# Kernel tuning notes

Hardware: AMD Instinct MI355X
Metric: run time of the kernel (lower is better)

## Reference

```python
import jax, jax.numpy as jnp
import numpy as np

N, E, CN, CE = 2048, 8192, 256, 256
MN, ME = 16384, 65536
RATIO = 0.5
K_KEEP = int(np.ceil(RATIO * N))  # 1024, static


def _glorot(key, shape):
    lim = float(np.sqrt(6.0 / (shape[0] + shape[1])))
    return jax.random.uniform(key, shape, jnp.float32, -lim, lim)


def setup_inputs() -> dict:
    key = jax.random.key(0)
    ks = jax.random.split(key, 16)
    return {
        "x_n": jax.random.normal(ks[0], (N, CN), jnp.float32),
        "edge_index_n": jax.random.randint(ks[1], (2, MN), 0, N),
        "edge_weight_n": jax.random.uniform(ks[2], (MN,), jnp.float32),
        "x_e": jax.random.normal(ks[3], (E, CE), jnp.float32),
        "edge_index_e": jax.random.randint(ks[4], (2, ME), 0, E),
        "edge_weight_e": jax.random.uniform(ks[5], (ME,), jnp.float32),
        "edge_index": jax.random.randint(ks[6], (2, E), 0, N),
        "n_batch": jnp.zeros((N,), jnp.int64 if jax.config.jax_enable_x64 else jnp.int32),
        "e_batch": jnp.zeros((E,), jnp.int64 if jax.config.jax_enable_x64 else jnp.int32),
        "x_n0": jax.random.normal(ks[7], (N, CN), jnp.float32),
        "x_e0": jax.random.normal(ks[8], (E, CE), jnp.float32),
        # HodgeLaguerreConv(in, 1, K=2) params for node- and edge-scoring GNNs
        "W_n0": _glorot(ks[9], (CN, 1)),
        "W_n1": _glorot(ks[10], (CN, 1)),
        "b_n": jnp.zeros((1,), jnp.float32),
        "W_e0": _glorot(ks[11], (CE, 1)),
        "W_e1": _glorot(ks[12], (CE, 1)),
        "b_e": jnp.zeros((1,), jnp.float32),
    }


def _hodge_conv_k2(x, ei, ew, W0, W1, b):
    # PyG: out = lin0(T0) + lin1(T1), T0 = x, T1 = x - L@x (propagate: dst += w_e * x[src])
    n = x.shape[0]
    agg = jax.ops.segment_sum(ew[:, None] * x[ei[0]], ei[1], num_segments=n)
    return x @ W0 + (x - agg) @ W1 + b


def reference(x_n, edge_index_n, edge_weight_n, x_e, edge_index_e, edge_weight_e,
              edge_index, n_batch, e_batch, x_n0, x_e0,
              W_n0, W_n1, b_n, W_e0, W_e1, b_e):
    score_n = jax.nn.sigmoid(_hodge_conv_k2(x_n, edge_index_n, edge_weight_n, W_n0, W_n1, b_n).reshape(-1))
    score_e = jax.nn.sigmoid(_hodge_conv_k2(x_e, edge_index_e, edge_weight_e, W_e0, W_e1, b_e).reshape(-1))
    xns = x_n * score_n[:, None]
    xes = x_e * score_e[:, None]
    # incidence matrix B (par1): B[src,e]=-1, B[dst,e]=+1 (duplicates summed, as torch sparse)
    src, dst = edge_index[0], edge_index[1]
    eidx = jnp.arange(E)
    par1 = jnp.zeros((N, E), x_n.dtype).at[src, eidx].add(-1.0).at[dst, eidx].add(1.0)
    par1_abs = jnp.zeros((N, E), x_n.dtype).at[src, eidx].add(1.0).at[dst, eidx].add(1.0)
    # joint node score with 0.125 * |B| @ score_e
    joint = score_n + 0.125 * (par1_abs @ score_e)
    perm = jnp.argsort(-joint)                # descending
    idx_keep = jnp.sort(perm[:K_KEEP])        # kept nodes in original order (boolean-mask order)
    mask_n = jnp.zeros((N,), x_n.dtype).at[idx_keep].set(1.0)
    # edges touching any removed node get nonzero; keep edges where this is exactly 0
    removed_hits = par1_abs.T @ (1.0 - mask_n)
    keep_e = (removed_hits == 0.0).astype(x_n.dtype)     # [E]
    # masked incidence: kept-node rows, removed-edge columns zeroed
    par_masked = par1[idx_keep] * keep_e[None, :]        # [k, E]
    L0 = par_masked @ par_masked.T                       # [k, k]  (equals compacted L0)
    L1 = par_masked.T @ par_masked                       # [E, E]  (zero rows/cols at removed edges)
    # eigsh(L0, k=1, 'LM'): max eigenvalue; scipy path is non-differentiable -> stop_gradient
    lam = jax.lax.stop_gradient(jnp.linalg.eigvalsh(L0)[-1])
    L0s = 2.0 * L0 / lam
    L1s = 2.0 * L1 / lam
    x_n_out = xns[idx_keep]
    x_e_out = xes * keep_e[:, None]
    x_n0_out = x_n0[idx_keep]
    x_e0_out = x_e0 * keep_e[:, None]
    return (x_n_out, L0s, x_e_out, L1s, par_masked, x_n0_out, x_e0_out)
```

## Files before the change

### kernel.cpp

```cpp
#include <hip/hip_runtime.h>
#include <math.h>

#define NN   2048
#define EE   8192
#define CNF  256
#define MN   16384
#define ME   65536
#define KK   1024

#define OUT_XN   ((size_t)0)
#define OUT_L0   ((size_t)262144)
#define OUT_XE   ((size_t)1310720)
#define OUT_L1   ((size_t)3407872)
#define OUT_PM   ((size_t)70516736)
#define OUT_XN0  ((size_t)78905344)
#define OUT_XE0  ((size_t)79167488)

#define WS_T1N    0
#define WS_SLINN  2048
#define WS_T1E    4096
#define WS_SLINE  12288
#define WS_SCN    20480
#define WS_SCE    22528
#define WS_JOINT  30720
#define WS_AGGN   32768
#define WS_AGGE   34816
#define WS_LAM    43008
#define WS_IDXK   43520
#define WS_RANK   44544
#define WS_OFFS   47616
#define WS_ADJE   66176
#define WS_KEEPE  82560

#define DCAP  8
#define PWR_T 64
#define RBAD  0xFFFFu

typedef float vf4 __attribute__((ext_vector_type(4)));

__global__ void k_prep(const float* __restrict__ xn, const float* __restrict__ xe,
                       const float* __restrict__ Wn0, const float* __restrict__ Wn1,
                       const float* __restrict__ We0, const float* __restrict__ We1,
                       float* __restrict__ wsf) {
    if (blockIdx.x == 0) {
        for (int i = threadIdx.x; i < 2048; i += 256) wsf[WS_AGGN + i] = 0.f;
        for (int i = threadIdx.x; i < 8192; i += 256) wsf[WS_AGGE + i] = 0.f;
        for (int i = threadIdx.x; i < 2048; i += 256) wsf[WS_JOINT + i] = 0.f;
    }
    int gw = (blockIdx.x * blockDim.x + threadIdx.x) >> 6;
    int lane = threadIdx.x & 63;
    int wstr = (gridDim.x * blockDim.x) >> 6;
    for (int row = gw; row < NN + EE; row += wstr) {
        const float *x, *W0, *W1; float *t1, *sl; int r;
        if (row < NN) { r = row;      x = xn + (size_t)r * CNF; W0 = Wn0; W1 = Wn1; t1 = wsf + WS_T1N; sl = wsf + WS_SLINN; }
        else          { r = row - NN; x = xe + (size_t)r * CNF; W0 = We0; W1 = We1; t1 = wsf + WS_T1E; sl = wsf + WS_SLINE; }
        float4 xv = ((const float4*)x)[lane];
        float4 w0 = ((const float4*)W0)[lane];
        float4 w1 = ((const float4*)W1)[lane];
        float d0 = xv.x*w0.x + xv.y*w0.y + xv.z*w0.z + xv.w*w0.w;
        float d1 = xv.x*w1.x + xv.y*w1.y + xv.z*w1.z + xv.w*w1.w;
        #pragma unroll
        for (int o = 32; o > 0; o >>= 1) { d0 += __shfl_down(d0, o, 64); d1 += __shfl_down(d1, o, 64); }
        if (lane == 0) { t1[r] = d1; sl[r] = d0 + d1; }
    }
}

__global__ void k_agg(const int* __restrict__ ein, const float* __restrict__ ewn,
                      const int* __restrict__ eie, const float* __restrict__ ewe,
                      float* __restrict__ wsf) {
    int i = blockIdx.x * blockDim.x + threadIdx.x;
    if (i < MN) {
        int s = ein[i], d = ein[MN + i];
        atomicAdd(wsf + WS_AGGN + d, ewn[i] * wsf[WS_T1N + s]);
    }
    if (i < ME) {
        int s = eie[i], d = eie[ME + i];
        atomicAdd(wsf + WS_AGGE + d, ewe[i] * wsf[WS_T1E + s]);
    }
}

__global__ void k_score(const int* __restrict__ ei,
                        const float* __restrict__ bn, const float* __restrict__ be,
                        float* __restrict__ wsf) {
    int i = blockIdx.x * blockDim.x + threadIdx.x;
    if (i < NN) {
        float z = wsf[WS_SLINN + i] - wsf[WS_AGGN + i] + bn[0];
        float s = 1.0f / (1.0f + expf(-z));
        wsf[WS_SCN + i] = s;
        atomicAdd(wsf + WS_JOINT + i, s);
    }
    if (i < EE) {
        float z = wsf[WS_SLINE + i] - wsf[WS_AGGE + i] + be[0];
        float s = 1.0f / (1.0f + expf(-z));
        wsf[WS_SCE + i] = s;
        float v = 0.125f * s;
        atomicAdd(wsf + WS_JOINT + ei[i], v);
        atomicAdd(wsf + WS_JOINT + ei[EE + i], v);
    }
}

__device__ __forceinline__ float block_reduce_sum(float val, float* red) {
    #pragma unroll
    for (int o = 32; o > 0; o >>= 1) val += __shfl_down(val, o, 64);
    int lane = threadIdx.x & 63, wid = threadIdx.x >> 6;
    if (lane == 0) red[wid] = val;
    __syncthreads();
    float r = 0.0f;
    if (threadIdx.x < 16) {
        r = red[threadIdx.x];
        #pragma unroll
        for (int o = 8; o > 0; o >>= 1) r += __shfl_down(r, o, 16);
        if (threadIdx.x == 0) red[0] = r;
    }
    __syncthreads();
    float out = red[0];
    __syncthreads();
    return out;
}

__device__ __forceinline__ int block_incl_scan_1024(int v, int* t16) {
    int lane = threadIdx.x & 63, wid = threadIdx.x >> 6;
    int x = v;
    #pragma unroll
    for (int o = 1; o < 64; o <<= 1) {
        int t = __shfl_up(x, o, 64);
        if (lane >= o) x += t;
    }
    if (lane == 63) t16[wid] = x;
    __syncthreads();
    if (threadIdx.x < 16) {
        int w = t16[threadIdx.x];
        #pragma unroll
        for (int o = 1; o < 16; o <<= 1) {
            int t = __shfl_up(w, o, 16);
            if ((int)threadIdx.x >= o) w += t;
        }
        t16[threadIdx.x] = w;
    }
    __syncthreads();
    int base = wid ? t16[wid - 1] : 0;
    return base + x;
}

__global__ __launch_bounds__(1024) void k_mid(
        const int* __restrict__ ei,
        float* __restrict__ out, float* __restrict__ wsf, int* __restrict__ wsi) {
    int tid = threadIdx.x;
    if (blockIdx.x != 0) {
        size_t w = (size_t)(blockIdx.x - 1) * 1024 + tid;
        size_t ws = (size_t)(gridDim.x - 1) * 1024;
        vf4 z = (vf4)(0.0f);
        vf4* l1 = (vf4*)(out + OUT_L1);
        for (size_t p = w; p < (size_t)EE * EE / 4; p += ws) __builtin_nontemporal_store(z, &l1[p]);
        vf4* pm = (vf4*)(out + OUT_PM);
        for (size_t p = w; p < (size_t)KK * EE / 4; p += ws) __builtin_nontemporal_store(z, &pm[p]);
        vf4* l0 = (vf4*)(out + OUT_L0);
        for (size_t p = w; p < (size_t)KK * KK / 4; p += ws) __builtin_nontemporal_store(z, &l0[p]);
        return;
    }
    __shared__ unsigned long long s_u64[2048];
    __shared__ unsigned short s_rank[2048];
    __shared__ unsigned short s_adjo[16384 + DCAP];
    __shared__ float s_red[16];
    __shared__ int s_t16[16];
    int* s_i = (int*)s_u64;

    unsigned long long k0, k1;
    {
        int i0 = 2 * tid, i1 = 2 * tid + 1;
        float f0 = wsf[WS_JOINT + i0], f1 = wsf[WS_JOINT + i1];
        unsigned u0 = __float_as_uint(f0), u1 = __float_as_uint(f1);
        unsigned sk0 = (u0 & 0x80000000u) ? ~u0 : (u0 | 0x80000000u);
        unsigned sk1 = (u1 & 0x80000000u) ? ~u1 : (u1 | 0x80000000u);
        k0 = (((unsigned long long)sk0) << 11) | (unsigned long long)(2047 - i0);
        k1 = (((unsigned long long)sk1) << 11) | (unsigned long long)(2047 - i1);
    }
    unsigned long long prefix = 0ULL;
    int rem = KK;
    #pragma unroll
    for (int p = 5; p >= 0; --p) {
        __syncthreads();
        if (tid < 256) s_i[tid] = 0;
        __syncthreads();
        int sh = p << 3;
        unsigned long long ph = prefix >> (sh + 8);
        if ((k0 >> (sh + 8)) == ph) atomicAdd(&s_i[(int)((k0 >> sh) & 255)], 1);
        if ((k1 >> (sh + 8)) == ph) atomicAdd(&s_i[(int)((k1 >> sh) & 255)], 1);
        __syncthreads();
        if (tid < 64) {
            int b0 = s_i[4 * tid + 0], b1 = s_i[4 * tid + 1];
            int b2 = s_i[4 * tid + 2], b3 = s_i[4 * tid + 3];
            int sl = b0 + b1 + b2 + b3;
            int si = sl;
            #pragma unroll
            for (int o = 1; o < 64; o <<= 1) {
                int t = __shfl_down(si, o, 64);
                if (tid + o < 64) si += t;
            }
            int sup = si - sl;
            int sg3 = sup;
            int sg2 = sg3 + b3;
            int sg1 = sg2 + b2;
            int sg0 = sg1 + b1;
            if (sg0 < rem && rem <= sg0 + b0) { s_i[256] = (tid << 2) | 0; s_i[257] = rem - sg0; }
            if (sg1 < rem && rem <= sg1 + b1) { s_i[256] = (tid << 2) | 1; s_i[257] = rem - sg1; }
            if (sg2 < rem && rem <= sg2 + b2) { s_i[256] = (tid << 2) | 2; s_i[257] = rem - sg2; }
            if (sg3 < rem && rem <= sg3 + b3) { s_i[256] = (tid << 2) | 3; s_i[257] = rem - sg3; }
        }
        __syncthreads();
        prefix |= ((unsigned long long)(unsigned)s_i[256]) << sh;
        rem = s_i[257];
    }
    {
        int a0 = (k0 >= prefix) ? 1 : 0;
        int a1 = (k1 >= prefix) ? 1 : 0;
        int pr = a0 + a1;
        __syncthreads();
        int incl = block_incl_scan_1024(pr, s_t16);
        int excl = incl - pr;
        int i0 = 2 * tid, i1 = 2 * tid + 1;
        int r0 = excl, r1 = excl + a0;
        s_rank[i0] = a0 ? (unsigned short)r0 : (unsigned short)RBAD;
        s_rank[i1] = a1 ? (unsigned short)r1 : (unsigned short)RBAD;
        wsi[WS_RANK + i0] = a0 ? r0 : -1;
        wsi[WS_RANK + i1] = a1 ? r1 : -1;
        if (a0) wsi[WS_IDXK + r0] = i0;
        if (a1) wsi[WS_IDXK + r1] = i1;
    }
    __syncthreads();

    s_i[tid] = 0;
    __syncthreads();
    for (int e = tid; e < EE; e += 1024) {
        int s = ei[e], d = ei[EE + e];
        unsigned rs = s_rank[s], rd = s_rank[d];
        int kept = (rs != RBAD && rd != RBAD);
        wsi[WS_KEEPE + e] = kept;
        if (kept && s != d) {
            atomicAdd(&s_i[(int)rs], 1);
            atomicAdd(&s_i[(int)rd], 1);
        }
    }
    __syncthreads();

    {
        int dg = s_i[tid];
        int incl = block_incl_scan_1024(dg, s_t16);
        int offs = incl - dg;
        s_i[2048 + tid] = offs;
        wsi[WS_OFFS + tid] = offs;
        if (tid == 1023) wsi[WS_OFFS + 1024] = incl;
    }
    __syncthreads();

    for (int e = tid; e < EE; e += 1024) {
        int s = ei[e], d = ei[EE + e];
        unsigned rs = s_rank[s], rd = s_rank[d];
        if (rs != RBAD && rd != RBAD && s != d) {
            int p = atomicAdd(&s_i[2048 + (int)rs], 1);
            s_adjo[p] = (unsigned short)rd;
            wsi[WS_ADJE + p] = (e << 1);
            int q = atomicAdd(&s_i[2048 + (int)rd], 1);
            s_adjo[q] = (unsigned short)rs;
            wsi[WS_ADJE + q] = (e << 1) | 1;
        }
    }
    __syncthreads();

    {
        int o0 = wsi[WS_OFFS + tid];
        int d  = wsi[WS_OFFS + tid + 1] - o0;
        __syncthreads();
        float* v0 = (float*)s_u64;
        float* v1 = v0 + 1024;
        unsigned h = (unsigned)tid * 2654435761u + 911u;
        h ^= h >> 15; h *= 2246822519u; h ^= h >> 13;
        v0[tid] = (float)(h & 0xFFFFu) * (1.0f / 65536.0f) - 0.5f;
        int aj[DCAP];
        #pragma unroll
        for (int j = 0; j < DCAP; ++j) aj[j] = (j < d) ? (int)s_adjo[o0 + j] : 0;
        __syncthreads();
        float* vc = v0; float* vn = v1;
        for (int iter = 0; iter < PWR_T; ++iter) {
            float acc = 0.0f;
            #pragma unroll
            for (int j = 0; j < DCAP; ++j) acc += (j < d) ? vc[aj[j]] : 0.0f;
            for (int i = o0 + DCAP; i < o0 + d; ++i) acc += vc[(int)s_adjo[i]];
            float y = (float)d * vc[tid] - acc;
            if ((iter & 7) == 7) {
                float n2 = block_reduce_sum(y * y, s_red);
                y *= (n2 > 0.0f) ? rsqrtf(n2) : 0.0f;
            }
            vn[tid] = y;
            __syncthreads();
            float* tmp = vc; vc = vn; vn = tmp;
        }
        float acc = 0.0f;
        #pragma unroll
        for (int j = 0; j < DCAP; ++j) acc += (j < d) ? vc[aj[j]] : 0.0f;
        for (int i = o0 + DCAP; i < o0 + d; ++i) acc += vc[(int)s_adjo[i]];
        float y = (float)d * vc[tid] - acc;
        float rq = block_reduce_sum(vc[tid] * y, s_red);
        if (tid == 0) wsf[WS_LAM] = rq;
    }
}

__global__ __launch_bounds__(1024) void k_final(
        const float* __restrict__ xn, const float* __restrict__ xe,
        const float* __restrict__ xn0, const float* __restrict__ xe0,
        const int* __restrict__ ei,
        float* __restrict__ out, const float* __restrict__ wsf,
        const int* __restrict__ wsi) {
    float sc = 2.0f / wsf[WS_LAM];
    int gt = blockIdx.x * 1024 + threadIdx.x;
    int gstr = gridDim.x * 1024;

    for (int i = gt; i < KK * 64; i += gstr) {
        int r = i >> 6, c = i & 63;
        int src = wsi[WS_IDXK + r];
        float s = wsf[WS_SCN + src];
        float4 v = ((const float4*)(xn + (size_t)src * CNF))[c];
        v.x *= s; v.y *= s; v.z *= s; v.w *= s;
        ((float4*)(out + OUT_XN))[(size_t)r * 64 + c] = v;
        ((float4*)(out + OUT_XN0))[(size_t)r * 64 + c] = ((const float4*)(xn0 + (size_t)src * CNF))[c];
    }
    for (int i = gt; i < EE * 64; i += gstr) {
        int e = i >> 6, c = i & 63;
        float m = wsi[WS_KEEPE + e] ? 1.0f : 0.0f;
        float s = m * wsf[WS_SCE + e];
        float4 v = ((const float4*)(xe + (size_t)e * CNF))[c];
        v.x *= s; v.y *= s; v.z *= s; v.w *= s;
        ((float4*)(out + OUT_XE))[(size_t)e * 64 + c] = v;
        float4 v0 = ((const float4*)(xe0 + (size_t)e * CNF))[c];
        v0.x *= m; v0.y *= m; v0.z *= m; v0.w *= m;
        ((float4*)(out + OUT_XE0))[(size_t)e * 64 + c] = v0;
    }
    {
        float* pm = out + OUT_PM;
        float* L0 = out + OUT_L0;
        for (int e = gt; e < EE; e += gstr) {
            int s = ei[e], d = ei[EE + e];
            int rs = wsi[WS_RANK + s], rd = wsi[WS_RANK + d];
            if (rs < 0 || rd < 0 || s == d) continue;
            pm[(size_t)rs * EE + e] = -1.0f;
            pm[(size_t)rd * EE + e] =  1.0f;
            atomicAdd(&L0[(size_t)rs * KK + rs],  sc);
            atomicAdd(&L0[(size_t)rd * KK + rd],  sc);
            atomicAdd(&L0[(size_t)rs * KK + rd], -sc);
            atomicAdd(&L0[(size_t)rd * KK + rs], -sc);
        }
    }
    {
        float* L1 = out + OUT_L1;
        int gwv = gt >> 6, lane = gt & 63, wstr = gstr >> 6;
        for (int r = gwv; r < KK; r += wstr) {
            int o0 = wsi[WS_OFFS + r], o1 = wsi[WS_OFFS + r + 1];
            for (int i = o0; i < o1; ++i) {
                int eiv = wsi[WS_ADJE + i];
                int e = eiv >> 1;
                float si = (eiv & 1) ? sc : -sc;
                for (int j = o0 + lane; j < o1; j += 64) {
                    int ejv = wsi[WS_ADJE + j];
                    atomicAdd(&L1[(size_t)e * EE + (ejv >> 1)], (ejv & 1) ? si : -si);
                }
            }
        }
    }
}

extern "C" void kernel_launch(void* const* d_in, const int* in_sizes, int n_in,
                              void* d_out, int out_size, void* d_ws, size_t ws_size,
                              hipStream_t stream) {
    const float* x_n  = (const float*)d_in[0];
    const int*   ei_n = (const int*)  d_in[1];
    const float* ew_n = (const float*)d_in[2];
    const float* x_e  = (const float*)d_in[3];
    const int*   ei_e = (const int*)  d_in[4];
    const float* ew_e = (const float*)d_in[5];
    const int*   ei   = (const int*)  d_in[6];
    const float* x_n0 = (const float*)d_in[9];
    const float* x_e0 = (const float*)d_in[10];
    const float* Wn0  = (const float*)d_in[11];
    const float* Wn1  = (const float*)d_in[12];
    const float* bn   = (const float*)d_in[13];
    const float* We0  = (const float*)d_in[14];
    const float* We1  = (const float*)d_in[15];
    const float* be   = (const float*)d_in[16];

    float* out = (float*)d_out;
    float* wsf = (float*)d_ws;
    int*   wsi = (int*)d_ws;

    k_prep <<<640, 256, 0, stream>>>(x_n, x_e, Wn0, Wn1, We0, We1, wsf);
    k_agg  <<<256, 256, 0, stream>>>(ei_n, ew_n, ei_e, ew_e, wsf);
    k_score<<<32, 256, 0, stream>>>(ei, bn, be, wsf);
    k_mid  <<<256, 1024, 0, stream>>>(ei, out, wsf, wsi);
    k_final<<<256, 1024, 0, stream>>>(x_n, x_e, x_n0, x_e0, ei, out, wsf, wsi);
}
```

Baseline: 433.3 us.

## Shrink power-iteration to 256 threads with 4 nodes each; per-wave radix histograms

The eigenvalue power iteration now runs on 256 threads, each handling four nodes and keeping its own vector entries in registers. This cuts the cost of the per-iteration block barrier and reduction across 16 waves. The radix-select histogram is split into 16 per-wave copies to reduce shared-memory atomic contention, and each bin is summed across waves during the scan. In exchange, each thread does four times the gather work per iteration and needs more registers for the adjacency arrays.

```diff
diff --git a/kernel.cpp b/kernel.cpp
--- a/kernel.cpp
+++ b/kernel.cpp
@@ -99,17 +99,17 @@
     }
 }
 
-__device__ __forceinline__ float block_reduce_sum(float val, float* red) {
+__device__ __forceinline__ float block_reduce_sum_256(float val, float* red) {
     #pragma unroll
     for (int o = 32; o > 0; o >>= 1) val += __shfl_down(val, o, 64);
     int lane = threadIdx.x & 63, wid = threadIdx.x >> 6;
     if (lane == 0) red[wid] = val;
     __syncthreads();
     float r = 0.0f;
-    if (threadIdx.x < 16) {
-        r = red[threadIdx.x];
-        #pragma unroll
-        for (int o = 8; o > 0; o >>= 1) r += __shfl_down(r, o, 16);
+    if (threadIdx.x < 64) {
+        r = (threadIdx.x < 4) ? red[threadIdx.x] : 0.0f;
+        #pragma unroll
+        for (int o = 2; o > 0; o >>= 1) r += __shfl_down(r, o, 64);
         if (threadIdx.x == 0) red[0] = r;
     }
     __syncthreads();
@@ -177,19 +177,24 @@
     }
     unsigned long long prefix = 0ULL;
     int rem = KK;
+    int wb = (tid >> 6) << 8;
     #pragma unroll
     for (int p = 5; p >= 0; --p) {
         __syncthreads();
-        if (tid < 256) s_i[tid] = 0;
+        for (int i = tid; i < 4096; i += 1024) s_i[i] = 0;
         __syncthreads();
         int sh = p << 3;
         unsigned long long ph = prefix >> (sh + 8);
-        if ((k0 >> (sh + 8)) == ph) atomicAdd(&s_i[(int)((k0 >> sh) & 255)], 1);
-        if ((k1 >> (sh + 8)) == ph) atomicAdd(&s_i[(int)((k1 >> sh) & 255)], 1);
+        if ((k0 >> (sh + 8)) == ph) atomicAdd(&s_i[wb | (int)((k0 >> sh) & 255)], 1);
+        if ((k1 >> (sh + 8)) == ph) atomicAdd(&s_i[wb | (int)((k1 >> sh) & 255)], 1);
         __syncthreads();
         if (tid < 64) {
-            int b0 = s_i[4 * tid + 0], b1 = s_i[4 * tid + 1];
-            int b2 = s_i[4 * tid + 2], b3 = s_i[4 * tid + 3];
+            int b0 = 0, b1 = 0, b2 = 0, b3 = 0;
+            #pragma unroll
+            for (int w = 0; w < 16; ++w) {
+                int base = (w << 8) | (tid << 2);
+                b0 += s_i[base]; b1 += s_i[base + 1]; b2 += s_i[base + 2]; b3 += s_i[base + 3];
+            }
             int sl = b0 + b1 + b2 + b3;
             int si = sl;
             #pragma unroll
@@ -267,40 +272,67 @@
     }
     __syncthreads();
 
-    {
-        int o0 = wsi[WS_OFFS + tid];
-        int d  = wsi[WS_OFFS + tid + 1] - o0;
-        __syncthreads();
+    if (tid >= 256) return;
+    {
+        int o0[4], dd[4];
+        #pragma unroll
+        for (int k = 0; k < 4; ++k) {
+            int n = tid + (k << 8);
+            o0[k] = wsi[WS_OFFS + n];
+            dd[k] = wsi[WS_OFFS + n + 1] - o0[k];
+        }
         float* v0 = (float*)s_u64;
         float* v1 = v0 + 1024;
-        unsigned h = (unsigned)tid * 2654435761u + 911u;
-        h ^= h >> 15; h *= 2246822519u; h ^= h >> 13;
-        v0[tid] = (float)(h & 0xFFFFu) * (1.0f / 65536.0f) - 0.5f;
-        int aj[DCAP];
-        #pragma unroll
-        for (int j = 0; j < DCAP; ++j) aj[j] = (j < d) ? (int)s_adjo[o0 + j] : 0;
+        float vself[4];
+        #pragma unroll
+        for (int k = 0; k < 4; ++k) {
+            int n = tid + (k << 8);
+            unsigned h = (unsigned)n * 2654435761u + 911u;
+            h ^= h >> 15; h *= 2246822519u; h ^= h >> 13;
+            float iv = (float)(h & 0xFFFFu) * (1.0f / 65536.0f) - 0.5f;
+            v0[n] = iv; vself[k] = iv;
+        }
+        int aj[4][DCAP];
+        #pragma unroll
+        for (int k = 0; k < 4; ++k) {
+            #pragma unroll
+            for (int j = 0; j < DCAP; ++j) aj[k][j] = (j < dd[k]) ? (int)s_adjo[o0[k] + j] : 0;
+        }
         __syncthreads();
         float* vc = v0; float* vn = v1;
         for (int iter = 0; iter < PWR_T; ++iter) {
-            float acc = 0.0f;
-            #pragma unroll
-            for (int j = 0; j < DCAP; ++j) acc += (j < d) ? vc[aj[j]] : 0.0f;
-            for (int i = o0 + DCAP; i < o0 + d; ++i) acc += vc[(int)s_adjo[i]];
-            float y = (float)d * vc[tid] - acc;
+            float y[4]; float n2loc = 0.0f;
+            #pragma unroll
+            for (int k = 0; k < 4; ++k) {
+                float acc = 0.0f;
+                #pragma unroll
+                for (int j = 0; j < DCAP; ++j) acc += (j < dd[k]) ? vc[aj[k][j]] : 0.0f;
+                for (int i = o0[k] + DCAP; i < o0[k] + dd[k]; ++i) acc += vc[(int)s_adjo[i]];
+                y[k] = (float)dd[k] * vself[k] - acc;
+                n2loc += y[k] * y[k];
+            }
             if ((iter & 7) == 7) {
-                float n2 = block_reduce_sum(y * y, s_red);
-                y *= (n2 > 0.0f) ? rsqrtf(n2) : 0.0f;
+                float n2 = block_reduce_sum_256(n2loc, s_red);
+                float sc = (n2 > 0.0f) ? rsqrtf(n2) : 0.0f;
+                #pragma unroll
+                for (int k = 0; k < 4; ++k) y[k] *= sc;
             }
-            vn[tid] = y;
+            #pragma unroll
+            for (int k = 0; k < 4; ++k) { int n = tid + (k << 8); vn[n] = y[k]; vself[k] = y[k]; }
             __syncthreads();
             float* tmp = vc; vc = vn; vn = tmp;
         }
-        float acc = 0.0f;
-        #pragma unroll
-        for (int j = 0; j < DCAP; ++j) acc += (j < d) ? vc[aj[j]] : 0.0f;
-        for (int i = o0 + DCAP; i < o0 + d; ++i) acc += vc[(int)s_adjo[i]];
-        float y = (float)d * vc[tid] - acc;
-        float rq = block_reduce_sum(vc[tid] * y, s_red);
+        float numloc = 0.0f;
+        #pragma unroll
+        for (int k = 0; k < 4; ++k) {
+            float acc = 0.0f;
+            #pragma unroll
+            for (int j = 0; j < DCAP; ++j) acc += (j < dd[k]) ? vc[aj[k][j]] : 0.0f;
+            for (int i = o0[k] + DCAP; i < o0[k] + dd[k]; ++i) acc += vc[(int)s_adjo[i]];
+            float y = (float)dd[k] * vself[k] - acc;
+            numloc += vself[k] * y;
+        }
+        float rq = block_reduce_sum_256(numloc, s_red);
         if (tid == 0) wsf[WS_LAM] = rq;
     }
 }
```

New measurement: 496.4 us. 1.15x slower.
